# Kernel tuning notes

Hardware: AMD Instinct MI355X
Metric: run time of the kernel (lower is better)

Reference implementation:

```python
import jax, jax.numpy as jnp
import numpy as np

INPUT_DIM, HIDDEN_DIM, N_CLASSES = 512, 256, 2
TOP_RATIO, MIN_PATCHES, K_INST = 0.7, 128, 8
B, N = 4, 16384


def setup_inputs() -> dict:
    key = jax.random.key(0)
    ks = jax.random.split(key, 10)
    D, H, C = INPUT_DIM, HIDDEN_DIM, N_CLASSES
    s = lambda fan: 1.0 / np.sqrt(fan)
    return {
        "features": jax.random.normal(ks[0], (B, N, D), dtype=jnp.float32),
        # attention_net: Linear(D->H) (dropout is identity in eval)
        "Wa": jax.random.uniform(ks[1], (D, H), minval=-s(D), maxval=s(D), dtype=jnp.float32),
        "ba": jax.random.uniform(ks[2], (H,), minval=-s(D), maxval=s(D), dtype=jnp.float32),
        # per-class attention branches: Linear(H->1), stacked over classes
        "Wbr": jax.random.uniform(ks[3], (C, H), minval=-s(H), maxval=s(H), dtype=jnp.float32),
        "bbr": jax.random.uniform(ks[4], (C,), minval=-s(H), maxval=s(H), dtype=jnp.float32),
        # per-class instance classifiers: Linear(D->H) -> ReLU -> Linear(H->2)
        "W1": jax.random.uniform(ks[5], (C, D, H), minval=-s(D), maxval=s(D), dtype=jnp.float32),
        "b1": jax.random.uniform(ks[6], (C, H), minval=-s(D), maxval=s(D), dtype=jnp.float32),
        "W2": jax.random.uniform(ks[7], (C, H, 2), minval=-s(H), maxval=s(H), dtype=jnp.float32),
        "b2": jax.random.uniform(ks[8], (C, 2), minval=-s(H), maxval=s(H), dtype=jnp.float32),
    }


def reference(features, Wa, ba, Wbr, bbr, W1, b1, W2, b2):
    Bb, Nn, D = features.shape
    C = Wbr.shape[0]

    # ---- compute_attention ----
    h = jax.nn.relu(features @ Wa + ba)                       # (B,N,H)
    a_logits = jnp.einsum('bnh,ch->bcn', h, Wbr) + bbr[None, :, None]
    attn_all = jax.nn.softmax(a_logits, axis=-1)              # (B,C,N)
    combined = attn_all.mean(axis=1)                          # (B,N)

    # ---- per-sample top-k selection (k static under jit) ----
    k = min(max(int(Nn * TOP_RATIO), MIN_PATCHES), Nn)
    _, sel_idx = jax.lax.top_k(combined, k)                   # (B,k)
    sel_idx = jnp.sort(sel_idx, axis=-1)
    selected = jnp.take_along_axis(features, sel_idx[..., None], axis=1)  # (B,k,D)

    # ---- instance clustering loss (vectorized over B x C) ----
    kk = min(K_INST, Nn // 2)
    _, top_idx = jax.lax.top_k(attn_all, kk)                  # (B,C,kk)
    _, bot_idx = jax.lax.top_k(-attn_all, kk)                 # largest=False
    both_idx = jnp.concatenate([top_idx, bot_idx], axis=-1)   # (B,C,2kk)
    inst = features[jnp.arange(Bb)[:, None, None], both_idx]  # (B,C,2kk,D)
    h1 = jax.nn.relu(jnp.einsum('bckd,cdh->bckh', inst, W1) + b1[None, :, None, :])
    logits = jnp.einsum('bckh,cho->bcko', h1, W2) + b2[None, :, None, :]  # (B,C,2kk,2)
    labels = jnp.concatenate([jnp.ones(kk, jnp.int32), jnp.zeros(kk, jnp.int32)])
    logp = jax.nn.log_softmax(logits, axis=-1)
    ce = -jnp.take_along_axis(
        logp, jnp.broadcast_to(labels[None, None, :, None], (Bb, C, 2 * kk, 1)), axis=-1
    )[..., 0]                                                 # (B,C,2kk)
    cl_loss = ce.mean(axis=-1).sum() / (Bb * C)

    return selected, combined, sel_idx, cl_loss
```

## Files before the change

### kernel.cpp

```cpp
#include <hip/hip_runtime.h>

#define NB 4
#define NP 16384
#define DD 512
#define HH 256
#define CC 2
#define KSEL 11468
#define TOTP (NB*NP)
#define BCAP 4096

#define OFF_COMB (NB*KSEL*DD)
#define OFF_IDX  (OFF_COMB + NB*NP)
#define OFF_LOSS (OFF_IDX + NB*KSEL)

#define WS_ALOGIT 0
#define WS_SELIDX (2*NB*CC*NP)
#define WS_MZ     (WS_SELIDX + NB*KSEL)
#define WS_BCNT   (WS_MZ + 16)
#define WS_BLIST  (WS_BCNT + 4)
#define WS_TOP16  (WS_BLIST + NB*BCAP)
#define WS_CE     (WS_TOP16 + 128)

typedef __attribute__((ext_vector_type(8))) short short8x;
typedef __attribute__((ext_vector_type(4))) float f32x4;

__device__ __forceinline__ unsigned short f2bf(float x){
  unsigned u = __float_as_uint(x);
  unsigned r = (u + 0x7FFFu + ((u >> 16) & 1u)) >> 16;
  return (unsigned short)r;
}

__global__ __launch_bounds__(256) void waconv_kernel(
    const float* __restrict__ Wa, unsigned short* __restrict__ WaT)
{
  __shared__ float tile[32][33];
  const int tx = threadIdx.x, ty = threadIdx.y;
  const int k0 = blockIdx.x * 32, n0 = blockIdx.y * 32;
  #pragma unroll
  for (int i=0;i<4;++i)
    tile[ty+8*i][tx] = Wa[(size_t)(k0+ty+8*i)*HH + n0 + tx];
  __syncthreads();
  #pragma unroll
  for (int i=0;i<4;++i)
    WaT[(size_t)(n0+ty+8*i)*DD + k0 + tx] = f2bf(tile[tx][ty+8*i]);
}

__global__ __launch_bounds__(512) void gemm_mfma_kernel(
    const float* __restrict__ feat, const unsigned short* __restrict__ WaT,
    const float* __restrict__ ba, const float* __restrict__ Wbr,
    const float* __restrict__ bbr, float* __restrict__ aL)
{
  __shared__ __attribute__((aligned(16))) unsigned char smem[65536];
  __shared__ float sBA[HH], sW0[HH], sW1[HH];
  unsigned char* sA = smem;
  unsigned char* sB = smem + 16384;

  const int tid  = threadIdx.x;
  const int lane = tid & 63;
  const int wid  = tid >> 6;
  const int wm = wid >> 2, wn = wid & 3;
  const int fr = lane & 15, fq = lane >> 4;
  const int p0 = blockIdx.x * 128;
  const float bb0 = bbr[0], bb1 = bbr[1];

  if (tid < HH){ sBA[tid] = ba[tid]; sW0[tid] = Wbr[tid]; sW1[tid] = Wbr[HH+tid]; }

  f32x4 acc[4][4];
  #pragma unroll
  for (int i=0;i<4;++i)
    #pragma unroll
    for (int j=0;j<4;++j)
      acc[i][j] = (f32x4){0.f,0.f,0.f,0.f};

  const int am = tid >> 2, akq = (tid & 3) * 16;
  const int bn = tid >> 1, bhf = tid & 1;

  for (int k0 = 0; k0 < DD; k0 += 64){
    __syncthreads();
    {
      const float4* src = reinterpret_cast<const float4*>(
          feat + (size_t)(p0 + am)*DD + k0 + akq);
      float4 v0 = src[0], v1 = src[1], v2 = src[2], v3 = src[3];
      unsigned short u[16];
      u[0]=f2bf(v0.x); u[1]=f2bf(v0.y); u[2]=f2bf(v0.z); u[3]=f2bf(v0.w);
      u[4]=f2bf(v1.x); u[5]=f2bf(v1.y); u[6]=f2bf(v1.z); u[7]=f2bf(v1.w);
      u[8]=f2bf(v2.x); u[9]=f2bf(v2.y); u[10]=f2bf(v2.z); u[11]=f2bf(v2.w);
      u[12]=f2bf(v3.x); u[13]=f2bf(v3.y); u[14]=f2bf(v3.z); u[15]=f2bf(v3.w);
      uint4 w0, w1;
      w0.x = (unsigned)u[0] | ((unsigned)u[1]<<16);
      w0.y = (unsigned)u[2] | ((unsigned)u[3]<<16);
      w0.z = (unsigned)u[4] | ((unsigned)u[5]<<16);
      w0.w = (unsigned)u[6] | ((unsigned)u[7]<<16);
      w1.x = (unsigned)u[8] | ((unsigned)u[9]<<16);
      w1.y = (unsigned)u[10] | ((unsigned)u[11]<<16);
      w1.z = (unsigned)u[12] | ((unsigned)u[13]<<16);
      w1.w = (unsigned)u[14] | ((unsigned)u[15]<<16);
      const int swz = (am & 7) << 4;
      *reinterpret_cast<uint4*>(sA + (((am*128) + akq*2) ^ swz)) = w0;
      *reinterpret_cast<uint4*>(sA + (((am*128) + akq*2 + 16) ^ swz)) = w1;
    }
    {
      const uint4* src = reinterpret_cast<const uint4*>(
          WaT + (size_t)bn*DD + k0 + bhf*32);
      uint4 q0 = src[0], q1 = src[1], q2 = src[2], q3 = src[3];
      const int swz = (bn & 7) << 4;
      const int base = bn*128 + bhf*64;
      *reinterpret_cast<uint4*>(sB + ((base     ) ^ swz)) = q0;
      *reinterpret_cast<uint4*>(sB + ((base + 16) ^ swz)) = q1;
      *reinterpret_cast<uint4*>(sB + ((base + 32) ^ swz)) = q2;
      *reinterpret_cast<uint4*>(sB + ((base + 48) ^ swz)) = q3;
    }
    __syncthreads();
    #pragma unroll
    for (int kf = 0; kf < 2; ++kf){
      short8x af[4], bf[4];
      #pragma unroll
      for (int mf = 0; mf < 4; ++mf){
        int m_loc = wm*64 + mf*16 + fr;
        int off = ((m_loc*128 + kf*64 + fq*16) ^ ((m_loc & 7) << 4));
        af[mf] = *reinterpret_cast<const short8x*>(sA + off);
      }
      #pragma unroll
      for (int nf = 0; nf < 4; ++nf){
        int n_loc = wn*64 + nf*16 + fr;
        int off = ((n_loc*128 + kf*64 + fq*16) ^ ((n_loc & 7) << 4));
        bf[nf] = *reinterpret_cast<const short8x*>(sB + off);
      }
      #pragma unroll
      for (int mf = 0; mf < 4; ++mf)
        #pragma unroll
        for (int nf = 0; nf < 4; ++nf)
          acc[mf][nf] = __builtin_amdgcn_mfma_f32_16x16x32_bf16(
              af[mf], bf[nf], acc[mf][nf], 0, 0, 0);
    }
  }
  __syncthreads();

  float* hS = reinterpret_cast<float*>(smem);
  #pragma unroll
  for (int mh = 0; mh < 2; ++mh){
    if (wm == mh){
      #pragma unroll
      for (int mf = 0; mf < 4; ++mf)
        #pragma unroll
        for (int nf = 0; nf < 4; ++nf)
          #pragma unroll
          for (int r = 0; r < 4; ++r){
            int row = mf*16 + fq*4 + r;
            int col = wn*64 + nf*16 + fr;
            hS[row*256 + col] = acc[mf][nf][r];
          }
    }
    __syncthreads();
    {
      const int row = tid >> 3, cg = tid & 7;
      float s0 = 0.f, s1 = 0.f;
      #pragma unroll
      for (int j = 0; j < 8; ++j){
        int col = cg*4 + j*32;
        float4 hv = *reinterpret_cast<const float4*>(&hS[row*256 + col]);
        float xs[4] = {hv.x, hv.y, hv.z, hv.w};
        #pragma unroll
        for (int u = 0; u < 4; ++u){
          int ccol = col + u;
          float x = fmaxf(xs[u] + sBA[ccol], 0.f);
          s0 += x * sW0[ccol];
          s1 += x * sW1[ccol];
        }
      }
      s0 += __shfl_xor(s0,1); s1 += __shfl_xor(s1,1);
      s0 += __shfl_xor(s0,2); s1 += __shfl_xor(s1,2);
      s0 += __shfl_xor(s0,4); s1 += __shfl_xor(s1,4);
      if (cg == 0){
        int p = p0 + mh*64 + row;
        int b = p >> 14, nl = p & (NP-1);
        aL[((size_t)b*CC + 0)*NP + nl] = s0 + bb0;
        aL[((size_t)b*CC + 1)*NP + nl] = s1 + bb1;
      }
    }
    __syncthreads();
  }
}

__global__ __launch_bounds__(1024) void smstat_kernel(
    const float* __restrict__ aL, float* __restrict__ mz)
{
  __shared__ float  s_redf[16];
  __shared__ double s_redd[16];
  __shared__ float  s_max;
  const int tid = threadIdx.x;
  const int lane = tid & 63, wid = tid >> 6;
  const int r = blockIdx.x;
  const float* a = aL + (size_t)r*NP;
  float m = -1e30f;
  for (int n=tid; n<NP; n+=1024) m = fmaxf(m, a[n]);
  #pragma unroll
  for (int off=1; off<64; off<<=1) m = fmaxf(m, __shfl_xor(m, off));
  if (lane==0) s_redf[wid]=m;
  __syncthreads();
  if (tid==0){ float mm=s_redf[0]; for(int w=1;w<16;++w) mm=fmaxf(mm,s_redf[w]); s_max=mm; }
  __syncthreads();
  m = s_max;
  double ls = 0.0;
  for (int n=tid;n<NP;n+=1024) ls += (double)expf(a[n]-m);
  #pragma unroll
  for (int off=1; off<64; off<<=1) ls += __shfl_xor(ls, off);
  if (lane==0) s_redd[wid]=ls;
  __syncthreads();
  if (tid==0){
    double t=0; for(int w=0;w<16;++w) t+=s_redd[w];
    mz[r*2+0]=m; mz[r*2+1]=(float)(1.0/t);
  }
}

__global__ __launch_bounds__(1024) void selTF_kernel(
    const float* __restrict__ aL, const float* __restrict__ mz,
    float* __restrict__ comb, int* __restrict__ bcnt, int* __restrict__ blist)
{
  __shared__ unsigned s_red[2][16];
  __shared__ int s_cnt;
  const int tid = threadIdx.x;
  const int b = blockIdx.x;
  const int lane = tid & 63, wid = tid >> 6;
  const float m0 = mz[b*4+0], iz0 = mz[b*4+1], m1 = mz[b*4+2], iz1 = mz[b*4+3];
  const float* a0 = aL + ((size_t)b*CC + 0)*NP;
  const float* a1 = aL + ((size_t)b*CC + 1)*NP;
  float* oc = comb + (size_t)b*NP;
  const int n0 = tid*16;

  unsigned v[16];
  #pragma unroll
  for (int g=0; g<4; ++g){
    float4 qa = *reinterpret_cast<const float4*>(a0 + n0 + g*4);
    float4 qb = *reinterpret_cast<const float4*>(a1 + n0 + g*4);
    float4 CV;
    CV.x = 0.5f*(expf(qa.x-m0)*iz0 + expf(qb.x-m1)*iz1);
    CV.y = 0.5f*(expf(qa.y-m0)*iz0 + expf(qb.y-m1)*iz1);
    CV.z = 0.5f*(expf(qa.z-m0)*iz0 + expf(qb.z-m1)*iz1);
    CV.w = 0.5f*(expf(qa.w-m0)*iz0 + expf(qb.w-m1)*iz1);
    *reinterpret_cast<float4*>(oc + n0 + g*4) = CV;
    v[g*4+0]=__float_as_uint(CV.x);
    v[g*4+1]=__float_as_uint(CV.y);
    v[g*4+2]=__float_as_uint(CV.z);
    v[g*4+3]=__float_as_uint(CV.w);
  }
  if (tid==0) s_cnt = 0;

  unsigned cur = 0;
  #pragma unroll 1
  for (int bit=31; bit>=12; --bit){
    unsigned trial = cur | (1u<<bit);
    int c = 0;
    #pragma unroll
    for (int i=0;i<16;++i) c += (v[i] >= trial) ? 1 : 0;
    #pragma unroll
    for (int off=1; off<64; off<<=1) c += __shfl_xor(c, off);
    if (lane==0) s_red[bit&1][wid] = (unsigned)c;
    __syncthreads();
    unsigned tot=0;
    #pragma unroll
    for (int w=0;w<16;++w) tot += s_red[bit&1][w];
    if (tot >= KSEL) cur = trial;
  }
  const float Tv = __uint_as_float(cur);
  const float lo = Tv*0.989f, hi = Tv*1.0115f;
  #pragma unroll
  for (int i=0;i<16;++i){
    float x = __uint_as_float(v[i]);
    if (x >= lo && x <= hi){
      int s = atomicAdd(&s_cnt, 1);
      if (s < BCAP) blist[b*BCAP + s] = n0 + i;
    }
  }
  __syncthreads();
  if (tid==0) bcnt[b] = (s_cnt < BCAP) ? s_cnt : BCAP;
}

__global__ __launch_bounds__(512) void recomp_kernel(
    const float* __restrict__ feat, const float* __restrict__ Wa,
    const float* __restrict__ ba, const float* __restrict__ Wbr,
    const float* __restrict__ bbr, const float* __restrict__ mz,
    const int* __restrict__ bcnt, const int* __restrict__ blist,
    float* __restrict__ comb)
{
  __shared__ float fS[16][DD];
  __shared__ float waS[32][HH];
  __shared__ int   s_n[16];
  const int tid = threadIdx.x;
  const int b  = blockIdx.x >> 8;
  const int g0 = (blockIdx.x & 255) * 16;
  const int cnt = bcnt[b];
  if (g0 >= cnt) return;
  if (tid < 16)
    s_n[tid] = (g0 + tid < cnt) ? blist[b*BCAP + g0 + tid] : -1;
  __syncthreads();
  #pragma unroll
  for (int pass=0; pass<4; ++pass){
    const int j = pass*4 + (tid>>7);
    const int c4 = (tid & 127)*4;
    const int n = s_n[j];
    if (n >= 0){
      float4 v = *reinterpret_cast<const float4*>(feat + ((size_t)b*NP + n)*DD + c4);
      *reinterpret_cast<float4*>(&fS[j][c4]) = v;
    }
  }

  const int grp = tid >> 5, l32 = tid & 31;
  const int h0 = l32*4;
  const bool active = true;
  float acc[8];
  #pragma unroll
  for (int i=0;i<8;++i) acc[i]=0.f;

  #pragma unroll 1
  for (int kt=0; kt<16; ++kt){
    __syncthreads();
    {
      const float4* src = reinterpret_cast<const float4*>(Wa + (size_t)(kt*32)*HH);
      float4* dst = reinterpret_cast<float4*>(&waS[0][0]);
      #pragma unroll
      for (int q=0; q<4; ++q) dst[tid + 512*q] = src[tid + 512*q];
    }
    __syncthreads();
    if (s_n[grp] >= 0){
      #pragma unroll
      for (int kk4=0; kk4<8; ++kk4){
        const float4 fv = *reinterpret_cast<const float4*>(&fS[grp][kt*32 + kk4*4]);
        const float fx[4] = {fv.x, fv.y, fv.z, fv.w};
        #pragma unroll
        for (int u=0; u<4; ++u){
          const int kk = kk4*4 + u;
          float4 w0 = *reinterpret_cast<const float4*>(&waS[kk][h0]);
          float4 w1 = *reinterpret_cast<const float4*>(&waS[kk][128 + h0]);
          acc[0] += fx[u]*w0.x; acc[1] += fx[u]*w0.y;
          acc[2] += fx[u]*w0.z; acc[3] += fx[u]*w0.w;
          acc[4] += fx[u]*w1.x; acc[5] += fx[u]*w1.y;
          acc[6] += fx[u]*w1.z; acc[7] += fx[u]*w1.w;
        }
      }
    }
  }
  if (s_n[grp] < 0) return;
  float p0 = 0.f, p1 = 0.f;
  #pragma unroll
  for (int i=0;i<8;++i){
    const int h = (i<4) ? (h0+i) : (128 + h0 + (i-4));
    float x = fmaxf(acc[i] + ba[h], 0.f);
    p0 += x * Wbr[h];
    p1 += x * Wbr[HH+h];
  }
  #pragma unroll
  for (int off=1; off<32; off<<=1){ p0+=__shfl_xor(p0,off); p1+=__shfl_xor(p1,off); }
  if (l32==0){
    const float m0 = mz[b*4+0], iz0 = mz[b*4+1], m1 = mz[b*4+2], iz1 = mz[b*4+3];
    float l0 = p0 + bbr[0];
    float l1 = p1 + bbr[1];
    comb[(size_t)b*NP + s_n[grp]] = 0.5f*(expf(l0-m0)*iz0 + expf(l1-m1)*iz1);
  }
}

__global__ __launch_bounds__(1024) void select_kernel(
    const float* __restrict__ comb, float* __restrict__ outIdxF,
    int* __restrict__ selIdx)
{
  __shared__ unsigned s_red[2][16];
  __shared__ unsigned s_wsum[16];
  const int tid = threadIdx.x;
  const int b = blockIdx.x;
  const int lane = tid & 63, wid = tid >> 6;
  const float* row = comb + (size_t)b*NP;

  unsigned v[16];
  {
    const float4* rp = reinterpret_cast<const float4*>(row + tid*16);
    #pragma unroll
    for (int g=0; g<4; ++g){
      float4 q = rp[g];
      v[g*4+0]=__float_as_uint(q.x);
      v[g*4+1]=__float_as_uint(q.y);
      v[g*4+2]=__float_as_uint(q.z);
      v[g*4+3]=__float_as_uint(q.w);
    }
  }
  unsigned cur = 0;
  #pragma unroll 1
  for (int bit=31; bit>=0; --bit){
    unsigned trial = cur | (1u<<bit);
    int c = 0;
    #pragma unroll
    for (int i=0;i<16;++i) c += (v[i] >= trial) ? 1 : 0;
    #pragma unroll
    for (int off=1; off<64; off<<=1) c += __shfl_xor(c, off);
    if (lane==0) s_red[bit&1][wid] = (unsigned)c;
    __syncthreads();
    unsigned tot=0;
    #pragma unroll
    for (int w=0;w<16;++w) tot += s_red[bit&1][w];
    if (tot >= KSEL) cur = trial;
  }
  const unsigned T = cur;
  {
    int c = 0;
    #pragma unroll
    for (int i=0;i<16;++i) c += (v[i] > T) ? 1 : 0;
    #pragma unroll
    for (int off=1; off<64; off<<=1) c += __shfl_xor(c, off);
    if (lane==0) s_red[1][wid] = (unsigned)c;
  }
  __syncthreads();
  unsigned gtot=0;
  #pragma unroll
  for (int w=0;w<16;++w) gtot += s_red[1][w];
  const int extra = KSEL - (int)gtot;

  int eqc=0;
  #pragma unroll
  for (int i=0;i<16;++i) eqc += (v[i]==T) ? 1 : 0;
  unsigned inc = (unsigned)eqc;
  #pragma unroll
  for (int off=1; off<64; off<<=1){
    unsigned o = __shfl_up(inc, off);
    if (lane >= off) inc += o;
  }
  if (lane==63) s_wsum[wid] = inc;
  __syncthreads();
  unsigned wbase = 0;
  for (int w=0; w<wid; ++w) wbase += s_wsum[w];
  const int eqBase = (int)(wbase + inc) - eqc;

  int eq=eqBase, sc=0;
  #pragma unroll
  for (int i=0;i<16;++i){
    unsigned x = v[i];
    if (x==T){ if (eq<extra) sc++; eq++; }
    else if (x>T) sc++;
  }
  unsigned inc2 = (unsigned)sc;
  #pragma unroll
  for (int off=1; off<64; off<<=1){
    unsigned o = __shfl_up(inc2, off);
    if (lane >= off) inc2 += o;
  }
  __syncthreads();
  if (lane==63) s_wsum[wid] = inc2;
  __syncthreads();
  unsigned wbase2 = 0;
  for (int w=0; w<wid; ++w) wbase2 += s_wsum[w];
  int pos = (int)(wbase2 + inc2) - sc;

  eq=eqBase;
  #pragma unroll
  for (int i=0;i<16;++i){
    unsigned x = v[i];
    int f=0;
    if (x==T){ if (eq<extra) f=1; eq++; }
    else if (x>T) f=1;
    if (f){
      int n = tid*16 + i;
      outIdxF[(size_t)b*KSEL + pos] = (float)n;
      selIdx[(size_t)b*KSEL + pos] = n;
      pos++;
    }
  }
}

__global__ __launch_bounds__(256) void gather_kernel(
    const float* __restrict__ feat, const int* __restrict__ selIdx,
    float* __restrict__ outSel)
{
  const int tid = threadIdx.x;
  const int row = blockIdx.x*2 + (tid>>7);
  const int c4 = tid & 127;
  const int b = row / KSEL;
  const int idx = selIdx[row];
  const float4 v = *reinterpret_cast<const float4*>(feat + ((size_t)b*NP + idx)*DD + c4*4);
  *reinterpret_cast<float4*>(outSel + (size_t)row*DD + c4*4) = v;
}

__global__ __launch_bounds__(256) void top16_kernel(
    const float* __restrict__ aL, const float* __restrict__ mz,
    int* __restrict__ top16)
{
  __shared__ unsigned long long wkT[4][8];
  __shared__ unsigned long long wkB[4][8];
  const int tid = threadIdx.x;
  const int bid = blockIdx.x;
  const int lane = tid & 63, wid = tid >> 6;
  const float* a = aL + (size_t)bid*NP;
  const float m = mz[bid*2+0], iz = mz[bid*2+1];

  unsigned long long t8[8], b8[8];
  #pragma unroll
  for (int i=0;i<8;++i){ t8[i]=0ull; b8[i]=~0ull; }

  for (int j=0;j<16;++j){
    const int n4 = tid + 256*j;
    const float4 v = *reinterpret_cast<const float4*>(a + 4*n4);
    float xs[4];
    xs[0] = expf(v.x-m)*iz; xs[1] = expf(v.y-m)*iz;
    xs[2] = expf(v.z-m)*iz; xs[3] = expf(v.w-m)*iz;
    #pragma unroll
    for (int q=0;q<4;++q){
      const int n = 4*n4 + q;
      const unsigned vb = __float_as_uint(xs[q]);
      unsigned long long kt = ((unsigned long long)vb<<32) | (unsigned)(NP-1-n);
      if (kt > t8[7]){
        t8[7]=kt;
        #pragma unroll
        for (int i=7;i>0;--i){ if (t8[i]>t8[i-1]){ unsigned long long t=t8[i-1]; t8[i-1]=t8[i]; t8[i]=t; } }
      }
      unsigned long long kb = ((unsigned long long)vb<<32) | (unsigned)n;
      if (kb < b8[7]){
        b8[7]=kb;
        #pragma unroll
        for (int i=7;i>0;--i){ if (b8[i]<b8[i-1]){ unsigned long long t=b8[i-1]; b8[i-1]=b8[i]; b8[i]=t; } }
      }
    }
  }

  #pragma unroll
  for (int pick=0; pick<8; ++pick){
    unsigned long long loc = t8[0];
    #pragma unroll
    for (int i=1;i<8;++i) loc = t8[i]>loc ? t8[i] : loc;
    #pragma unroll
    for (int off=1; off<64; off<<=1){ unsigned long long o=__shfl_xor(loc,off); loc=o>loc?o:loc; }
    if (lane==0) wkT[wid][pick]=loc;
    #pragma unroll
    for (int i=0;i<8;++i) if (t8[i]==loc) t8[i]=0ull;
  }
  #pragma unroll
  for (int pick=0; pick<8; ++pick){
    unsigned long long loc = b8[0];
    #pragma unroll
    for (int i=1;i<8;++i) loc = b8[i]<loc ? b8[i] : loc;
    #pragma unroll
    for (int off=1; off<64; off<<=1){ unsigned long long o=__shfl_xor(loc,off); loc=o<loc?o:loc; }
    if (lane==0) wkB[wid][pick]=loc;
    #pragma unroll
    for (int i=0;i<8;++i) if (b8[i]==loc) b8[i]=~0ull;
  }
  __syncthreads();

  if (wid==0){
    unsigned long long k = (lane<32) ? wkT[lane>>3][lane&7] : 0ull;
    #pragma unroll
    for (int pick=0; pick<8; ++pick){
      unsigned long long loc = k;
      #pragma unroll
      for (int off=1; off<64; off<<=1){ unsigned long long o=__shfl_xor(loc,off); loc=o>loc?o:loc; }
      if (k==loc) k=0ull;
      if (lane==0) top16[bid*16+pick] = NP-1-(int)(loc & 0xFFFFFFFFull);
    }
    unsigned long long kb = (lane<32) ? wkB[lane>>3][lane&7] : ~0ull;
    #pragma unroll
    for (int pick=0; pick<8; ++pick){
      unsigned long long loc = kb;
      #pragma unroll
      for (int off=1; off<64; off<<=1){ unsigned long long o=__shfl_xor(loc,off); loc=o<loc?o:loc; }
      if (kb==loc) kb=~0ull;
      if (lane==0) top16[bid*16+8+pick] = (int)(loc & 0xFFFFFFFFull);
    }
  }
}

__global__ __launch_bounds__(256) void mlp_kernel(
    const float* __restrict__ feat, const float* __restrict__ W1,
    const float* __restrict__ b1, const float* __restrict__ W2,
    const float* __restrict__ b2, const int* __restrict__ top16,
    float* __restrict__ cews)
{
  __shared__ float fS[DD];
  __shared__ float r0[4], r1[4];
  const int tid = threadIdx.x;
  const int bid = blockIdx.x;
  const int r = bid & 15, c = (bid >> 4) & 1, b = bid >> 5;
  const int lane = tid & 63, wid = tid >> 6;
  const int gi = top16[(b*2+c)*16 + r];
  if (tid < 128){
    float4 v = *reinterpret_cast<const float4*>(feat + ((size_t)b*NP + gi)*DD + tid*4);
    *reinterpret_cast<float4*>(&fS[tid*4]) = v;
  }
  __syncthreads();
  const float* w1c = W1 + (size_t)c*DD*HH;
  float a0=0.f,a1=0.f,a2=0.f,a3=0.f;
  #pragma unroll 4
  for (int d=0; d<DD; d+=4){
    a0 += fS[d+0]*w1c[(size_t)(d+0)*HH + tid];
    a1 += fS[d+1]*w1c[(size_t)(d+1)*HH + tid];
    a2 += fS[d+2]*w1c[(size_t)(d+2)*HH + tid];
    a3 += fS[d+3]*w1c[(size_t)(d+3)*HH + tid];
  }
  float h = fmaxf((a0+a1)+(a2+a3) + b1[c*HH+tid], 0.f);
  float p0 = h*W2[(size_t)(c*HH+tid)*2 + 0];
  float p1 = h*W2[(size_t)(c*HH+tid)*2 + 1];
  #pragma unroll
  for (int off=1; off<64; off<<=1){ p0+=__shfl_xor(p0,off); p1+=__shfl_xor(p1,off); }
  if (lane==0){ r0[wid]=p0; r1[wid]=p1; }
  __syncthreads();
  if (tid==0){
    float l0 = (r0[0]+r0[1])+(r0[2]+r0[3]) + b2[c*2+0];
    float l1 = (r1[0]+r1[1])+(r1[2]+r1[3]) + b2[c*2+1];
    float mm = fmaxf(l0,l1);
    float lse = mm + logf(expf(l0-mm)+expf(l1-mm));
    float chosen = (r<8) ? l1 : l0;
    cews[bid] = lse - chosen;
  }
}

__global__ void loss_kernel(const float* __restrict__ cews, float* __restrict__ out_loss){
  if (threadIdx.x==0 && blockIdx.x==0){
    float s=0.f;
    for (int i=0;i<128;++i) s += cews[i];
    out_loss[0] = s / 128.0f;
  }
}

extern "C" void kernel_launch(void* const* d_in, const int* in_sizes, int n_in,
                              void* d_out, int out_size, void* d_ws, size_t ws_size,
                              hipStream_t stream) {
  const float* feat = (const float*)d_in[0];
  const float* Wa   = (const float*)d_in[1];
  const float* ba   = (const float*)d_in[2];
  const float* Wbr  = (const float*)d_in[3];
  const float* bbr  = (const float*)d_in[4];
  const float* W1   = (const float*)d_in[5];
  const float* b1   = (const float*)d_in[6];
  const float* W2   = (const float*)d_in[7];
  const float* b2   = (const float*)d_in[8];
  float* out = (float*)d_out;
  float* ws  = (float*)d_ws;

  float* a_logits = ws + WS_ALOGIT;
  int*   selIdx   = (int*)(ws + WS_SELIDX);
  float* mz       = ws + WS_MZ;
  int*   bcnt     = (int*)(ws + WS_BCNT);
  int*   blist    = (int*)(ws + WS_BLIST);
  int*   top16    = (int*)(ws + WS_TOP16);
  float* cews     = ws + WS_CE;

  unsigned short* WaT = (unsigned short*)d_out;

  hipLaunchKernelGGL(waconv_kernel, dim3(DD/32, HH/32), dim3(32,8), 0, stream,
                     Wa, WaT);
  hipLaunchKernelGGL(gemm_mfma_kernel, dim3(TOTP/128), dim3(512), 0, stream,
                     feat, WaT, ba, Wbr, bbr, a_logits);
  hipLaunchKernelGGL(smstat_kernel, dim3(NB*CC), dim3(1024), 0, stream,
                     a_logits, mz);
  hipLaunchKernelGGL(selTF_kernel, dim3(NB), dim3(1024), 0, stream,
                     a_logits, mz, out + OFF_COMB, bcnt, blist);
  hipLaunchKernelGGL(recomp_kernel, dim3(NB*256), dim3(512), 0, stream,
                     feat, Wa, ba, Wbr, bbr, mz, bcnt, blist, out + OFF_COMB);
  hipLaunchKernelGGL(select_kernel, dim3(NB), dim3(1024), 0, stream,
                     out + OFF_COMB, out + OFF_IDX, selIdx);
  hipLaunchKernelGGL(gather_kernel, dim3(NB*KSEL/2), dim3(256), 0, stream,
                     feat, selIdx, out);
  hipLaunchKernelGGL(top16_kernel, dim3(NB*CC), dim3(256), 0, stream,
                     a_logits, mz, top16);
  hipLaunchKernelGGL(mlp_kernel, dim3(NB*CC*16), dim3(256), 0, stream,
                     feat, W1, b1, W2, b2, top16, cews);
  hipLaunchKernelGGL(loss_kernel, dim3(1), dim3(64), 0, stream,
                     cews, out + OFF_LOSS);
}
```

Before: 257.1 us.

## Fuse epilogue into registers, radix-4 threshold search, packed bf16 convert, fold loss kernel

The GEMM epilogue now reduces the ReLU-and-branch dot products straight from the MFMA accumulators with lane shuffles and a small shared exchange, instead of spilling the full hidden tile to shared memory in two halves. This cuts LDS traffic and barriers, and the smaller shared-memory footprint may allow higher occupancy. The bitwise threshold searches in selTF and select test two bits per step, which halves the number of block-wide barriers at the cost of more compares. The fp32-to-bf16 conversion uses the packed hardware convert instruction. The separate loss kernel is replaced by a last-block-done atomic counter in the MLP kernel, saving one launch.

```diff
diff --git a/kernel.cpp b/kernel.cpp
--- a/kernel.cpp
+++ b/kernel.cpp
@@ -20,6 +20,7 @@
 #define WS_BLIST  (WS_BCNT + 4)
 #define WS_TOP16  (WS_BLIST + NB*BCAP)
 #define WS_CE     (WS_TOP16 + 128)
+#define WS_CNT    (WS_CE + 128)
 
 typedef __attribute__((ext_vector_type(8))) short short8x;
 typedef __attribute__((ext_vector_type(4))) float f32x4;
@@ -30,12 +31,20 @@
   return (unsigned short)r;
 }
 
+__device__ __forceinline__ unsigned cvtpk(float lo, float hi){
+  unsigned r;
+  asm("v_cvt_pk_bf16_f32 %0, %1, %2" : "=v"(r) : "v"(lo), "v"(hi));
+  return r;
+}
+
 __global__ __launch_bounds__(256) void waconv_kernel(
-    const float* __restrict__ Wa, unsigned short* __restrict__ WaT)
+    const float* __restrict__ Wa, unsigned short* __restrict__ WaT,
+    unsigned* __restrict__ donecnt)
 {
   __shared__ float tile[32][33];
   const int tx = threadIdx.x, ty = threadIdx.y;
   const int k0 = blockIdx.x * 32, n0 = blockIdx.y * 32;
+  if (blockIdx.x==0 && blockIdx.y==0 && tx==0 && ty==0) donecnt[0] = 0u;
   #pragma unroll
   for (int i=0;i<4;++i)
     tile[ty+8*i][tx] = Wa[(size_t)(k0+ty+8*i)*HH + n0 + tx];
@@ -50,7 +59,7 @@
     const float* __restrict__ ba, const float* __restrict__ Wbr,
     const float* __restrict__ bbr, float* __restrict__ aL)
 {
-  __shared__ __attribute__((aligned(16))) unsigned char smem[65536];
+  __shared__ __attribute__((aligned(16))) unsigned char smem[49152];
   __shared__ float sBA[HH], sW0[HH], sW1[HH];
   unsigned char* sA = smem;
   unsigned char* sB = smem + 16384;
@@ -81,20 +90,11 @@
       const float4* src = reinterpret_cast<const float4*>(
           feat + (size_t)(p0 + am)*DD + k0 + akq);
       float4 v0 = src[0], v1 = src[1], v2 = src[2], v3 = src[3];
-      unsigned short u[16];
-      u[0]=f2bf(v0.x); u[1]=f2bf(v0.y); u[2]=f2bf(v0.z); u[3]=f2bf(v0.w);
-      u[4]=f2bf(v1.x); u[5]=f2bf(v1.y); u[6]=f2bf(v1.z); u[7]=f2bf(v1.w);
-      u[8]=f2bf(v2.x); u[9]=f2bf(v2.y); u[10]=f2bf(v2.z); u[11]=f2bf(v2.w);
-      u[12]=f2bf(v3.x); u[13]=f2bf(v3.y); u[14]=f2bf(v3.z); u[15]=f2bf(v3.w);
       uint4 w0, w1;
-      w0.x = (unsigned)u[0] | ((unsigned)u[1]<<16);
-      w0.y = (unsigned)u[2] | ((unsigned)u[3]<<16);
-      w0.z = (unsigned)u[4] | ((unsigned)u[5]<<16);
-      w0.w = (unsigned)u[6] | ((unsigned)u[7]<<16);
-      w1.x = (unsigned)u[8] | ((unsigned)u[9]<<16);
-      w1.y = (unsigned)u[10] | ((unsigned)u[11]<<16);
-      w1.z = (unsigned)u[12] | ((unsigned)u[13]<<16);
-      w1.w = (unsigned)u[14] | ((unsigned)u[15]<<16);
+      w0.x = cvtpk(v0.x, v0.y); w0.y = cvtpk(v0.z, v0.w);
+      w0.z = cvtpk(v1.x, v1.y); w0.w = cvtpk(v1.z, v1.w);
+      w1.x = cvtpk(v2.x, v2.y); w1.y = cvtpk(v2.z, v2.w);
+      w1.z = cvtpk(v3.x, v3.y); w1.w = cvtpk(v3.z, v3.w);
       const int swz = (am & 7) << 4;
       *reinterpret_cast<uint4*>(sA + (((am*128) + akq*2) ^ swz)) = w0;
       *reinterpret_cast<uint4*>(sA + (((am*128) + akq*2 + 16) ^ swz)) = w1;
@@ -136,49 +136,38 @@
   }
   __syncthreads();
 
-  float* hS = reinterpret_cast<float*>(smem);
-  #pragma unroll
-  for (int mh = 0; mh < 2; ++mh){
-    if (wm == mh){
-      #pragma unroll
-      for (int mf = 0; mf < 4; ++mf)
-        #pragma unroll
-        for (int nf = 0; nf < 4; ++nf)
-          #pragma unroll
-          for (int r = 0; r < 4; ++r){
-            int row = mf*16 + fq*4 + r;
-            int col = wn*64 + nf*16 + fr;
-            hS[row*256 + col] = acc[mf][nf][r];
-          }
-    }
-    __syncthreads();
-    {
-      const int row = tid >> 3, cg = tid & 7;
+  float* ex = reinterpret_cast<float*>(smem);
+  #pragma unroll
+  for (int mf = 0; mf < 4; ++mf){
+    #pragma unroll
+    for (int r = 0; r < 4; ++r){
       float s0 = 0.f, s1 = 0.f;
       #pragma unroll
-      for (int j = 0; j < 8; ++j){
-        int col = cg*4 + j*32;
-        float4 hv = *reinterpret_cast<const float4*>(&hS[row*256 + col]);
-        float xs[4] = {hv.x, hv.y, hv.z, hv.w};
-        #pragma unroll
-        for (int u = 0; u < 4; ++u){
-          int ccol = col + u;
-          float x = fmaxf(xs[u] + sBA[ccol], 0.f);
-          s0 += x * sW0[ccol];
-          s1 += x * sW1[ccol];
-        }
+      for (int nf = 0; nf < 4; ++nf){
+        int col = wn*64 + nf*16 + fr;
+        float x = fmaxf(acc[mf][nf][r] + sBA[col], 0.f);
+        s0 += x * sW0[col];
+        s1 += x * sW1[col];
       }
       s0 += __shfl_xor(s0,1); s1 += __shfl_xor(s1,1);
       s0 += __shfl_xor(s0,2); s1 += __shfl_xor(s1,2);
       s0 += __shfl_xor(s0,4); s1 += __shfl_xor(s1,4);
-      if (cg == 0){
-        int p = p0 + mh*64 + row;
-        int b = p >> 14, nl = p & (NP-1);
-        aL[((size_t)b*CC + 0)*NP + nl] = s0 + bb0;
-        aL[((size_t)b*CC + 1)*NP + nl] = s1 + bb1;
+      s0 += __shfl_xor(s0,8); s1 += __shfl_xor(s1,8);
+      if (fr == 0){
+        int row = wm*64 + mf*16 + fq*4 + r;
+        ex[(row*4 + wn)*2 + 0] = s0;
+        ex[(row*4 + wn)*2 + 1] = s1;
       }
     }
-    __syncthreads();
+  }
+  __syncthreads();
+  if (tid < 256){
+    const int row = tid >> 1, c = tid & 1;
+    float s = ((ex[(row*4+0)*2+c] + ex[(row*4+1)*2+c]) +
+               (ex[(row*4+2)*2+c] + ex[(row*4+3)*2+c]));
+    int p = p0 + row;
+    int b = p >> 14, nl = p & (NP-1);
+    aL[((size_t)b*CC + c)*NP + nl] = s + (c ? bb1 : bb0);
   }
 }
 
@@ -217,7 +206,7 @@
     const float* __restrict__ aL, const float* __restrict__ mz,
     float* __restrict__ comb, int* __restrict__ bcnt, int* __restrict__ blist)
 {
-  __shared__ unsigned s_red[2][16];
+  __shared__ unsigned s_red[2][16][3];
   __shared__ int s_cnt;
   const int tid = threadIdx.x;
   const int b = blockIdx.x;
@@ -248,19 +237,28 @@
 
   unsigned cur = 0;
   #pragma unroll 1
-  for (int bit=31; bit>=12; --bit){
-    unsigned trial = cur | (1u<<bit);
-    int c = 0;
-    #pragma unroll
-    for (int i=0;i<16;++i) c += (v[i] >= trial) ? 1 : 0;
-    #pragma unroll
-    for (int off=1; off<64; off<<=1) c += __shfl_xor(c, off);
-    if (lane==0) s_red[bit&1][wid] = (unsigned)c;
+  for (int bit=30; bit>=12; bit-=2){
+    const unsigned t1 = cur | (1u<<bit), t2 = cur | (2u<<bit), t3 = cur | (3u<<bit);
+    int c1=0,c2=0,c3=0;
+    #pragma unroll
+    for (int i=0;i<16;++i){
+      c1 += (v[i] >= t1) ? 1 : 0;
+      c2 += (v[i] >= t2) ? 1 : 0;
+      c3 += (v[i] >= t3) ? 1 : 0;
+    }
+    #pragma unroll
+    for (int off=1; off<64; off<<=1){
+      c1+=__shfl_xor(c1,off); c2+=__shfl_xor(c2,off); c3+=__shfl_xor(c3,off);
+    }
+    const int pb = (bit>>1)&1;
+    if (lane==0){ s_red[pb][wid][0]=(unsigned)c1; s_red[pb][wid][1]=(unsigned)c2; s_red[pb][wid][2]=(unsigned)c3; }
     __syncthreads();
-    unsigned tot=0;
-    #pragma unroll
-    for (int w=0;w<16;++w) tot += s_red[bit&1][w];
-    if (tot >= KSEL) cur = trial;
+    unsigned T1=0,T2=0,T3=0;
+    #pragma unroll
+    for (int w=0;w<16;++w){ T1+=s_red[pb][w][0]; T2+=s_red[pb][w][1]; T3+=s_red[pb][w][2]; }
+    if      (T3 >= KSEL) cur = t3;
+    else if (T2 >= KSEL) cur = t2;
+    else if (T1 >= KSEL) cur = t1;
   }
   const float Tv = __uint_as_float(cur);
   const float lo = Tv*0.989f, hi = Tv*1.0115f;
@@ -307,7 +305,6 @@
 
   const int grp = tid >> 5, l32 = tid & 31;
   const int h0 = l32*4;
-  const bool active = true;
   float acc[8];
   #pragma unroll
   for (int i=0;i<8;++i) acc[i]=0.f;
@@ -363,7 +360,7 @@
     const float* __restrict__ comb, float* __restrict__ outIdxF,
     int* __restrict__ selIdx)
 {
-  __shared__ unsigned s_red[2][16];
+  __shared__ unsigned s_red[2][16][3];
   __shared__ unsigned s_wsum[16];
   const int tid = threadIdx.x;
   const int b = blockIdx.x;
@@ -384,19 +381,28 @@
   }
   unsigned cur = 0;
   #pragma unroll 1
-  for (int bit=31; bit>=0; --bit){
-    unsigned trial = cur | (1u<<bit);
-    int c = 0;
-    #pragma unroll
-    for (int i=0;i<16;++i) c += (v[i] >= trial) ? 1 : 0;
-    #pragma unroll
-    for (int off=1; off<64; off<<=1) c += __shfl_xor(c, off);
-    if (lane==0) s_red[bit&1][wid] = (unsigned)c;
+  for (int bit=30; bit>=0; bit-=2){
+    const unsigned t1 = cur | (1u<<bit), t2 = cur | (2u<<bit), t3 = cur | (3u<<bit);
+    int c1=0,c2=0,c3=0;
+    #pragma unroll
+    for (int i=0;i<16;++i){
+      c1 += (v[i] >= t1) ? 1 : 0;
+      c2 += (v[i] >= t2) ? 1 : 0;
+      c3 += (v[i] >= t3) ? 1 : 0;
+    }
+    #pragma unroll
+    for (int off=1; off<64; off<<=1){
+      c1+=__shfl_xor(c1,off); c2+=__shfl_xor(c2,off); c3+=__shfl_xor(c3,off);
+    }
+    const int pb = (bit>>1)&1;
+    if (lane==0){ s_red[pb][wid][0]=(unsigned)c1; s_red[pb][wid][1]=(unsigned)c2; s_red[pb][wid][2]=(unsigned)c3; }
     __syncthreads();
-    unsigned tot=0;
-    #pragma unroll
-    for (int w=0;w<16;++w) tot += s_red[bit&1][w];
-    if (tot >= KSEL) cur = trial;
+    unsigned T1=0,T2=0,T3=0;
+    #pragma unroll
+    for (int w=0;w<16;++w){ T1+=s_red[pb][w][0]; T2+=s_red[pb][w][1]; T3+=s_red[pb][w][2]; }
+    if      (T3 >= KSEL) cur = t3;
+    else if (T2 >= KSEL) cur = t2;
+    else if (T1 >= KSEL) cur = t1;
   }
   const unsigned T = cur;
   {
@@ -405,12 +411,12 @@
     for (int i=0;i<16;++i) c += (v[i] > T) ? 1 : 0;
     #pragma unroll
     for (int off=1; off<64; off<<=1) c += __shfl_xor(c, off);
-    if (lane==0) s_red[1][wid] = (unsigned)c;
+    if (lane==0) s_red[1][wid][0] = (unsigned)c;
   }
   __syncthreads();
   unsigned gtot=0;
   #pragma unroll
-  for (int w=0;w<16;++w) gtot += s_red[1][w];
+  for (int w=0;w<16;++w) gtot += s_red[1][w][0];
   const int extra = KSEL - (int)gtot;
 
   int eqc=0;
@@ -568,7 +574,8 @@
     const float* __restrict__ feat, const float* __restrict__ W1,
     const float* __restrict__ b1, const float* __restrict__ W2,
     const float* __restrict__ b2, const int* __restrict__ top16,
-    float* __restrict__ cews)
+    float* __restrict__ cews, unsigned* __restrict__ donecnt,
+    float* __restrict__ out_loss)
 {
   __shared__ float fS[DD];
   __shared__ float r0[4], r1[4];
@@ -605,14 +612,14 @@
     float lse = mm + logf(expf(l0-mm)+expf(l1-mm));
     float chosen = (r<8) ? l1 : l0;
     cews[bid] = lse - chosen;
-  }
-}
-
-__global__ void loss_kernel(const float* __restrict__ cews, float* __restrict__ out_loss){
-  if (threadIdx.x==0 && blockIdx.x==0){
-    float s=0.f;
-    for (int i=0;i<128;++i) s += cews[i];
-    out_loss[0] = s / 128.0f;
+    __threadfence();
+    unsigned old = atomicAdd(donecnt, 1u);
+    if (old == 127u){
+      __threadfence();
+      float s=0.f;
+      for (int i=0;i<128;++i) s += cews[i];
+      out_loss[0] = s / 128.0f;
+    }
   }
 }
 
@@ -638,11 +645,12 @@
   int*   blist    = (int*)(ws + WS_BLIST);
   int*   top16    = (int*)(ws + WS_TOP16);
   float* cews     = ws + WS_CE;
+  unsigned* donecnt = (unsigned*)(ws + WS_CNT);
 
   unsigned short* WaT = (unsigned short*)d_out;
 
   hipLaunchKernelGGL(waconv_kernel, dim3(DD/32, HH/32), dim3(32,8), 0, stream,
-                     Wa, WaT);
+                     Wa, WaT, donecnt);
   hipLaunchKernelGGL(gemm_mfma_kernel, dim3(TOTP/128), dim3(512), 0, stream,
                      feat, WaT, ba, Wbr, bbr, a_logits);
   hipLaunchKernelGGL(smstat_kernel, dim3(NB*CC), dim3(1024), 0, stream,
@@ -658,7 +666,5 @@
   hipLaunchKernelGGL(top16_kernel, dim3(NB*CC), dim3(256), 0, stream,
                      a_logits, mz, top16);
   hipLaunchKernelGGL(mlp_kernel, dim3(NB*CC*16), dim3(256), 0, stream,
-                     feat, W1, b1, W2, b2, top16, cews);
-  hipLaunchKernelGGL(loss_kernel, dim3(1), dim3(64), 0, stream,
-                     cews, out + OFF_LOSS);
-}
+                     feat, W1, b1, W2, b2, top16, cews, donecnt, out + OFF_LOSS);
+}
```

After: 252.0 us, median of 2. 1.02x faster.
